# Kernel optimization log

Measured on AMD Instinct MI355X. Metric: run time of the kernel, lower is better.

## Reference

```python
import jax, jax.numpy as jnp
import numpy as np
import math

B, N, H, D = 2, 2048, 16, 64

def setup_inputs() -> dict:
    key = jax.random.key(0)
    kq, kk, kv = jax.random.split(key, 3)
    q = jax.random.normal(kq, (B, N, H, D), dtype=jnp.float32)
    k = jax.random.normal(kk, (B, N, H, D), dtype=jnp.float32)
    v = jax.random.normal(kv, (B, N, H, D), dtype=jnp.float32)
    return {"q": q, "k": k, "v": v}

def reference(q, k, v):
    d = q.shape[-1]
    # [b,n,h,d] -> [b,h,n,d]
    qh = jnp.transpose(q, (0, 2, 1, 3))
    kh = jnp.transpose(k, (0, 2, 1, 3))
    vh = jnp.transpose(v, (0, 2, 1, 3))
    # scores: [b,h,n,n]
    scores = jnp.einsum('bhqd,bhkd->bhqk', qh, kh) / math.sqrt(d)
    # jax.nn.softmax performs the stable max-subtraction internally,
    # matching the original's explicit max-subtract + softmax.
    attn = jax.nn.softmax(scores, axis=-1)
    o = jnp.einsum('bhqk,bhkd->bhqd', attn, vh)
    # back to [b,n,h,d]
    return jnp.transpose(o, (0, 2, 1, 3))
```

## Files before the change

kernel.cpp:

```cpp
#include <hip/hip_runtime.h>


typedef float  f32x4  __attribute__((ext_vector_type(4)));
typedef float  f32x16 __attribute__((ext_vector_type(16)));
typedef short  s16x8  __attribute__((ext_vector_type(8)));
typedef short  s16x4  __attribute__((ext_vector_type(4)));
typedef int    i32x4  __attribute__((ext_vector_type(4)));

#define QSCALE 0.18033688011112042f

__device__ __forceinline__ unsigned short bf16r(float f) {
    unsigned u = __builtin_bit_cast(unsigned, f);
    u += 0x7fffu + ((u >> 16) & 1u);
    return (unsigned short)(u >> 16);
}

__device__ __forceinline__ s16x8 cvt8f_scaled(const float* p, float s) {
    f32x4 a = *(const f32x4*)p;
    f32x4 b = *(const f32x4*)(p + 4);
    s16x8 r;
#pragma unroll
    for (int i = 0; i < 4; ++i) {
        r[i]   = (short)bf16r(a[i] * s);
        r[i+4] = (short)bf16r(b[i] * s);
    }
    return r;
}

__device__ __forceinline__ int cvtpk2(float lo, float hi) {
    int r;
    asm("v_cvt_pk_bf16_f32 %0, %1, %2" : "=v"(r) : "v"(lo), "v"(hi));
    return r;
}

__device__ __forceinline__ void gll16(const unsigned short* g, short* l) {
    __builtin_amdgcn_global_load_lds(
        (const __attribute__((address_space(1))) unsigned int*)g,
        (__attribute__((address_space(3))) unsigned int*)l, 16, 0, 0);
}

__global__ void __launch_bounds__(256)
prep(const float* __restrict__ K, const float* __restrict__ V,
     unsigned short* __restrict__ Kt, unsigned short* __restrict__ Vt) {
    const int t = threadIdx.x, bid = blockIdx.x;
    const int bh = bid & 31, nb = bid >> 5;
    const int b = bh >> 4, h = bh & 15;
    const size_t tile0 = ((size_t)bh * 64 + nb * 2) * 2048;

#pragma unroll
    for (int i = 0; i < 2; ++i) {
        const int lin = i * 256 + t;
        const int kbl = lin >> 8, rem = lin & 255;
        const int kc = rem >> 6, l = rem & 63;
        const int nl = l & 31, gg = l >> 5;
        const float* src = K + ((size_t)(b * 2048 + nb * 64 + kbl * 32 + nl)) * 1024
                             + h * 64 + kc * 16 + gg * 8;
        f32x4 a = *(const f32x4*)src;
        f32x4 c = *(const f32x4*)(src + 4);
        i32x4 o = { cvtpk2(a[0], a[1]), cvtpk2(a[2], a[3]),
                    cvtpk2(c[0], c[1]), cvtpk2(c[2], c[3]) };
        *(i32x4*)(Kt + tile0 + kbl * 2048 + kc * 512 + l * 8) = o;
    }

#pragma unroll
    for (int i = 0; i < 2; ++i) {
        const int lin = i * 256 + t;
        const int kbl = lin >> 8, rem = lin & 255;
        const int qq = rem >> 6, l = rem & 63;
        const int dt = qq >> 1, s = qq & 1;
        const int nl = l & 31, gg = l >> 5;
        const float* vp0 = V + ((size_t)(b * 2048 + nb * 64 + kbl * 32 + 8 * s + 4 * gg)) * 1024
                             + h * 64 + dt * 32 + nl;
        float x0 = vp0[0],     x1 = vp0[1024],  x2 = vp0[2048],  x3 = vp0[3072];
        float x4 = vp0[16384], x5 = vp0[17408], x6 = vp0[18432], x7 = vp0[19456];
        i32x4 o = { cvtpk2(x0, x1), cvtpk2(x2, x3),
                    cvtpk2(x4, x5), cvtpk2(x6, x7) };
        *(i32x4*)(Vt + tile0 + kbl * 2048 + qq * 512 + l * 8) = o;
    }
}

__global__ void __launch_bounds__(256, 3)
attn_fwd(const float* __restrict__ Q, const unsigned short* __restrict__ Kt,
         const unsigned short* __restrict__ Vt, float* __restrict__ O)
{
    __shared__ __align__(16) char smem[52224];

    const int t = threadIdx.x;
    const int ksel = t >> 6, lane = t & 63;
    const int g = lane >> 5, nl = lane & 31;

    const int bid = blockIdx.x;
    const int bh  = bid & 31, qb = bid >> 5;
    const int b   = bh >> 4,  h  = bh & 15;
    const int q0  = qb * 64;

    s16x8 qf[2][4];
#pragma unroll
    for (int qt = 0; qt < 2; ++qt) {
        const float* qp = Q + ((size_t)(b * 2048 + q0 + qt * 32 + nl)) * 1024
                            + h * 64 + g * 8;
#pragma unroll
        for (int kc = 0; kc < 4; ++kc)
            qf[qt][kc] = cvt8f_scaled(qp + kc * 16, QSCALE);
    }
    asm volatile("s_waitcnt vmcnt(0)" ::: "memory");
    __builtin_amdgcn_sched_barrier(0);

    const unsigned short* gk = Kt + (size_t)bh * 131072 + (size_t)ksel * 32768 + lane * 8;
    const unsigned short* gv = Vt + (size_t)bh * 131072 + (size_t)ksel * 32768 + lane * 8;

    short* sK = (short*)(smem + ksel * 8192);
    short* sV = (short*)(smem + ksel * 8192 + 4096);

    f32x16 oa00 = {}, oa01 = {}, oa10 = {}, oa11 = {};
    f32x4  lpv0 = {}, lpv1 = {};

#define ISSUEK(IT) do { const unsigned short* _g = gk + (IT) * 2048;        \
        _Pragma("unroll")                                                   \
        for (int _i = 0; _i < 4; ++_i) gll16(_g + _i * 512, sK + _i * 512); \
        } while (0)
#define ISSUEV(IT) do { const unsigned short* _g = gv + (IT) * 2048;        \
        _Pragma("unroll")                                                   \
        for (int _i = 0; _i < 4; ++_i) gll16(_g + _i * 512, sV + _i * 512); \
        } while (0)
#define WAITV(N) do {                                                       \
        asm volatile("s_waitcnt vmcnt(" #N ")" ::: "memory");               \
        __builtin_amdgcn_sched_barrier(0); } while (0)
#define LGKM0 do {                                                          \
        asm volatile("s_waitcnt lgkmcnt(0)" ::: "memory");                  \
        __builtin_amdgcn_sched_barrier(0); } while (0)

    ISSUEK(0);
    ISSUEV(0);

#pragma unroll
    for (int it = 0; it < 16; ++it) {
        WAITV(4);
        s16x8 kf[4];
#pragma unroll
        for (int kc = 0; kc < 4; ++kc)
            kf[kc] = *(const s16x8*)&sK[kc * 512 + lane * 8];
        LGKM0;
        if (it < 15) ISSUEK(it + 1);

        f32x16 s0 = {}, s1 = {};
#pragma unroll
        for (int kc = 0; kc < 4; ++kc) {
            s0 = __builtin_amdgcn_mfma_f32_32x32x16_bf16(kf[kc], qf[0][kc], s0, 0, 0, 0);
            s1 = __builtin_amdgcn_mfma_f32_32x32x16_bf16(kf[kc], qf[1][kc], s1, 0, 0, 0);
        }
        int pk0[8], pk1[8];
#pragma unroll
        for (int c = 0; c < 4; ++c) {
            f32x4 e0 = { __builtin_amdgcn_exp2f(s0[4*c]),   __builtin_amdgcn_exp2f(s0[4*c+1]),
                         __builtin_amdgcn_exp2f(s0[4*c+2]), __builtin_amdgcn_exp2f(s0[4*c+3]) };
            f32x4 e1 = { __builtin_amdgcn_exp2f(s1[4*c]),   __builtin_amdgcn_exp2f(s1[4*c+1]),
                         __builtin_amdgcn_exp2f(s1[4*c+2]), __builtin_amdgcn_exp2f(s1[4*c+3]) };
            lpv0 += e0; lpv1 += e1;
            pk0[2*c]   = cvtpk2(e0[0], e0[1]);  pk0[2*c+1] = cvtpk2(e0[2], e0[3]);
            pk1[2*c]   = cvtpk2(e1[0], e1[1]);  pk1[2*c+1] = cvtpk2(e1[2], e1[3]);
        }

        if (it < 15) { WAITV(4); } else { WAITV(0); }
        s16x8 vf[4];
#pragma unroll
        for (int qq = 0; qq < 4; ++qq)
            vf[qq] = *(const s16x8*)&sV[qq * 512 + lane * 8];
        LGKM0;
        if (it < 15) ISSUEV(it + 1);

#pragma unroll
        for (int s = 0; s < 2; ++s) {
            i32x4 b0 = { pk0[s*2], pk0[s*2+1], pk0[s*2+4], pk0[s*2+5] };
            i32x4 b1 = { pk1[s*2], pk1[s*2+1], pk1[s*2+4], pk1[s*2+5] };
            s16x8 bb0 = __builtin_bit_cast(s16x8, b0);
            s16x8 bb1 = __builtin_bit_cast(s16x8, b1);
            oa00 = __builtin_amdgcn_mfma_f32_32x32x16_bf16(vf[s],     bb0, oa00, 0, 0, 0);
            oa10 = __builtin_amdgcn_mfma_f32_32x32x16_bf16(vf[2 + s], bb0, oa10, 0, 0, 0);
            oa01 = __builtin_amdgcn_mfma_f32_32x32x16_bf16(vf[s],     bb1, oa01, 0, 0, 0);
            oa11 = __builtin_amdgcn_mfma_f32_32x32x16_bf16(vf[2 + s], bb1, oa11, 0, 0, 0);
        }
    }

#undef ISSUEK
#undef ISSUEV
#undef WAITV
#undef LGKM0

    float lp[2] = { lpv0[0] + lpv0[1] + lpv0[2] + lpv0[3],
                    lpv1[0] + lpv1[1] + lpv1[2] + lpv1[3] };

    __syncthreads();
    float* ex = (float*)smem;
    if (ksel) {
        float* zone = ex + (ksel - 1) * (64 * 68) + lane * 68;
#pragma unroll
        for (int i = 0; i < 4; ++i) {
            *(f32x4*)(zone + i * 4) =
                (f32x4){ oa00[4*i], oa00[4*i+1], oa00[4*i+2], oa00[4*i+3] };
            *(f32x4*)(zone + 16 + i * 4) =
                (f32x4){ oa01[4*i], oa01[4*i+1], oa01[4*i+2], oa01[4*i+3] };
            *(f32x4*)(zone + 32 + i * 4) =
                (f32x4){ oa10[4*i], oa10[4*i+1], oa10[4*i+2], oa10[4*i+3] };
            *(f32x4*)(zone + 48 + i * 4) =
                (f32x4){ oa11[4*i], oa11[4*i+1], oa11[4*i+2], oa11[4*i+3] };
        }
        zone[64] = lp[0];
        zone[65] = lp[1];
    }
    __syncthreads();
    if (!ksel) {
        float lps0 = lp[0], lps1 = lp[1];
#pragma unroll
        for (int z = 0; z < 3; ++z) {
            const float* zn = ex + z * (64 * 68) + lane * 68;
#pragma unroll
            for (int i = 0; i < 4; ++i) {
                f32x4 u0 = *(const f32x4*)(zn + i * 4);
                f32x4 u1 = *(const f32x4*)(zn + 16 + i * 4);
                f32x4 u2 = *(const f32x4*)(zn + 32 + i * 4);
                f32x4 u3 = *(const f32x4*)(zn + 48 + i * 4);
#pragma unroll
                for (int j = 0; j < 4; ++j) {
                    oa00[4*i+j] += u0[j]; oa01[4*i+j] += u1[j];
                    oa10[4*i+j] += u2[j]; oa11[4*i+j] += u3[j];
                }
            }
            lps0 += zn[64];
            lps1 += zn[65];
        }
        float inv[2];
        {
            float ss0 = lps0 + __shfl_xor(lps0, 32);
            float ss1 = lps1 + __shfl_xor(lps1, 32);
            inv[0] = 1.0f / ss0;
            inv[1] = 1.0f / ss1;
        }
        float* op0 = O + ((size_t)(b * 2048 + q0 + nl)) * 1024 + h * 64;
        float* op1 = op0 + 32 * 1024;
#pragma unroll
        for (int rq = 0; rq < 4; ++rq) {
            const int d0 = 8 * rq + 4 * g;
            *(f32x4*)(op0 + d0) = (f32x4){
                oa00[4*rq]   * inv[0], oa00[4*rq+1] * inv[0],
                oa00[4*rq+2] * inv[0], oa00[4*rq+3] * inv[0] };
            *(f32x4*)(op0 + 32 + d0) = (f32x4){
                oa10[4*rq]   * inv[0], oa10[4*rq+1] * inv[0],
                oa10[4*rq+2] * inv[0], oa10[4*rq+3] * inv[0] };
            *(f32x4*)(op1 + d0) = (f32x4){
                oa01[4*rq]   * inv[1], oa01[4*rq+1] * inv[1],
                oa01[4*rq+2] * inv[1], oa01[4*rq+3] * inv[1] };
            *(f32x4*)(op1 + 32 + d0) = (f32x4){
                oa11[4*rq]   * inv[1], oa11[4*rq+1] * inv[1],
                oa11[4*rq+2] * inv[1], oa11[4*rq+3] * inv[1] };
        }
    }
}

extern "C" void kernel_launch(void* const* d_in, const int* in_sizes, int n_in,
                              void* d_out, int out_size, void* d_ws, size_t ws_size,
                              hipStream_t stream) {
    const float* q = (const float*)d_in[0];
    const float* k = (const float*)d_in[1];
    const float* v = (const float*)d_in[2];
    float* o = (float*)d_out;

    unsigned short* Kt = (unsigned short*)d_ws;
    unsigned short* Vt = Kt + 4194304;

    hipLaunchKernelGGL(prep,     dim3(1024), dim3(256), 0, stream, k, v, Kt, Vt);
    hipLaunchKernelGGL(attn_fwd, dim3(1024), dim3(256), 0, stream, q, Kt, Vt, o);
}
```

Baseline: 132.9 us.

## Load K/V fragments directly from global into registers with prefetch and setprio

Replaces the global_load_lds staging of K and V tiles through shared memory with direct global-to-register loads. The next tile is prefetched into registers during the MFMA and exp work, the loop is no longer unrolled, the two score MFMA chains are split into separate blocks, and s_setprio raises wave priority around the MFMA sections. This removes the LDS round trip and its explicit waitcnt fences. In exchange it relies on the compiler's waitcnt placement, increases register pressure, and drops the barrier before the epilogue reuses shared memory.

```diff
diff --git a/kernel.cpp b/kernel.cpp
--- a/kernel.cpp
+++ b/kernel.cpp
@@ -31,12 +31,6 @@
     int r;
     asm("v_cvt_pk_bf16_f32 %0, %1, %2" : "=v"(r) : "v"(lo), "v"(hi));
     return r;
-}
-
-__device__ __forceinline__ void gll16(const unsigned short* g, short* l) {
-    __builtin_amdgcn_global_load_lds(
-        (const __attribute__((address_space(1))) unsigned int*)g,
-        (__attribute__((address_space(3))) unsigned int*)l, 16, 0, 0);
 }
 
 __global__ void __launch_bounds__(256)
@@ -83,7 +77,7 @@
 attn_fwd(const float* __restrict__ Q, const unsigned short* __restrict__ Kt,
          const unsigned short* __restrict__ Vt, float* __restrict__ O)
 {
-    __shared__ __align__(16) char smem[52224];
+    __shared__ __align__(16) float ex[3 * 64 * 68];
 
     const int t = threadIdx.x;
     const int ksel = t >> 6, lane = t & 63;
@@ -103,72 +97,71 @@
         for (int kc = 0; kc < 4; ++kc)
             qf[qt][kc] = cvt8f_scaled(qp + kc * 16, QSCALE);
     }
-    asm volatile("s_waitcnt vmcnt(0)" ::: "memory");
-    __builtin_amdgcn_sched_barrier(0);
-
-    const unsigned short* gk = Kt + (size_t)bh * 131072 + (size_t)ksel * 32768 + lane * 8;
-    const unsigned short* gv = Vt + (size_t)bh * 131072 + (size_t)ksel * 32768 + lane * 8;
-
-    short* sK = (short*)(smem + ksel * 8192);
-    short* sV = (short*)(smem + ksel * 8192 + 4096);
+
+    const unsigned short* ka = Kt + (size_t)bh * 131072 + (size_t)ksel * 32768 + lane * 8;
+    const unsigned short* va = Vt + (size_t)bh * 131072 + (size_t)ksel * 32768 + lane * 8;
 
     f32x16 oa00 = {}, oa01 = {}, oa10 = {}, oa11 = {};
     f32x4  lpv0 = {}, lpv1 = {};
 
-#define ISSUEK(IT) do { const unsigned short* _g = gk + (IT) * 2048;        \
-        _Pragma("unroll")                                                   \
-        for (int _i = 0; _i < 4; ++_i) gll16(_g + _i * 512, sK + _i * 512); \
-        } while (0)
-#define ISSUEV(IT) do { const unsigned short* _g = gv + (IT) * 2048;        \
-        _Pragma("unroll")                                                   \
-        for (int _i = 0; _i < 4; ++_i) gll16(_g + _i * 512, sV + _i * 512); \
-        } while (0)
-#define WAITV(N) do {                                                       \
-        asm volatile("s_waitcnt vmcnt(" #N ")" ::: "memory");               \
-        __builtin_amdgcn_sched_barrier(0); } while (0)
-#define LGKM0 do {                                                          \
-        asm volatile("s_waitcnt lgkmcnt(0)" ::: "memory");                  \
-        __builtin_amdgcn_sched_barrier(0); } while (0)
-
-    ISSUEK(0);
-    ISSUEV(0);
-
-#pragma unroll
+    s16x8 kf[4], vf[4];
+
+#pragma unroll
+    for (int i = 0; i < 4; ++i) {
+        kf[i] = *(const s16x8*)(ka + i * 512);
+        vf[i] = *(const s16x8*)(va + i * 512);
+    }
+    const unsigned short* kp = ka + 2048;
+    const unsigned short* vp = va + 2048;
+
+#pragma unroll 1
     for (int it = 0; it < 16; ++it) {
-        WAITV(4);
-        s16x8 kf[4];
-#pragma unroll
-        for (int kc = 0; kc < 4; ++kc)
-            kf[kc] = *(const s16x8*)&sK[kc * 512 + lane * 8];
-        LGKM0;
-        if (it < 15) ISSUEK(it + 1);
-
-        f32x16 s0 = {}, s1 = {};
-#pragma unroll
-        for (int kc = 0; kc < 4; ++kc) {
-            s0 = __builtin_amdgcn_mfma_f32_32x32x16_bf16(kf[kc], qf[0][kc], s0, 0, 0, 0);
-            s1 = __builtin_amdgcn_mfma_f32_32x32x16_bf16(kf[kc], qf[1][kc], s1, 0, 0, 0);
-        }
         int pk0[8], pk1[8];
-#pragma unroll
-        for (int c = 0; c < 4; ++c) {
-            f32x4 e0 = { __builtin_amdgcn_exp2f(s0[4*c]),   __builtin_amdgcn_exp2f(s0[4*c+1]),
-                         __builtin_amdgcn_exp2f(s0[4*c+2]), __builtin_amdgcn_exp2f(s0[4*c+3]) };
-            f32x4 e1 = { __builtin_amdgcn_exp2f(s1[4*c]),   __builtin_amdgcn_exp2f(s1[4*c+1]),
-                         __builtin_amdgcn_exp2f(s1[4*c+2]), __builtin_amdgcn_exp2f(s1[4*c+3]) };
-            lpv0 += e0; lpv1 += e1;
-            pk0[2*c]   = cvtpk2(e0[0], e0[1]);  pk0[2*c+1] = cvtpk2(e0[2], e0[3]);
-            pk1[2*c]   = cvtpk2(e1[0], e1[1]);  pk1[2*c+1] = cvtpk2(e1[2], e1[3]);
-        }
-
-        if (it < 15) { WAITV(4); } else { WAITV(0); }
-        s16x8 vf[4];
-#pragma unroll
-        for (int qq = 0; qq < 4; ++qq)
-            vf[qq] = *(const s16x8*)&sV[qq * 512 + lane * 8];
-        LGKM0;
-        if (it < 15) ISSUEV(it + 1);
-
+
+        {
+            f32x16 sc = {};
+            __builtin_amdgcn_s_setprio(1);
+#pragma unroll
+            for (int kc = 0; kc < 4; ++kc)
+                sc = __builtin_amdgcn_mfma_f32_32x32x16_bf16(kf[kc], qf[0][kc], sc, 0, 0, 0);
+            __builtin_amdgcn_s_setprio(0);
+#pragma unroll
+            for (int c = 0; c < 4; ++c) {
+                f32x4 e = { __builtin_amdgcn_exp2f(sc[4*c]),
+                            __builtin_amdgcn_exp2f(sc[4*c+1]),
+                            __builtin_amdgcn_exp2f(sc[4*c+2]),
+                            __builtin_amdgcn_exp2f(sc[4*c+3]) };
+                lpv0 += e;
+                pk0[2*c]   = cvtpk2(e[0], e[1]);
+                pk0[2*c+1] = cvtpk2(e[2], e[3]);
+            }
+        }
+
+        {
+            f32x16 sc = {};
+            __builtin_amdgcn_s_setprio(1);
+#pragma unroll
+            for (int kc = 0; kc < 4; ++kc)
+                sc = __builtin_amdgcn_mfma_f32_32x32x16_bf16(kf[kc], qf[1][kc], sc, 0, 0, 0);
+            __builtin_amdgcn_s_setprio(0);
+            if (it < 15) {
+#pragma unroll
+                for (int i = 0; i < 4; ++i)
+                    kf[i] = *(const s16x8*)(kp + i * 512);
+            }
+#pragma unroll
+            for (int c = 0; c < 4; ++c) {
+                f32x4 e = { __builtin_amdgcn_exp2f(sc[4*c]),
+                            __builtin_amdgcn_exp2f(sc[4*c+1]),
+                            __builtin_amdgcn_exp2f(sc[4*c+2]),
+                            __builtin_amdgcn_exp2f(sc[4*c+3]) };
+                lpv1 += e;
+                pk1[2*c]   = cvtpk2(e[0], e[1]);
+                pk1[2*c+1] = cvtpk2(e[2], e[3]);
+            }
+        }
+
+        __builtin_amdgcn_s_setprio(1);
 #pragma unroll
         for (int s = 0; s < 2; ++s) {
             i32x4 b0 = { pk0[s*2], pk0[s*2+1], pk0[s*2+4], pk0[s*2+5] };
@@ -180,18 +173,19 @@
             oa01 = __builtin_amdgcn_mfma_f32_32x32x16_bf16(vf[s],     bb1, oa01, 0, 0, 0);
             oa11 = __builtin_amdgcn_mfma_f32_32x32x16_bf16(vf[2 + s], bb1, oa11, 0, 0, 0);
         }
-    }
-
-#undef ISSUEK
-#undef ISSUEV
-#undef WAITV
-#undef LGKM0
+        __builtin_amdgcn_s_setprio(0);
+        if (it < 15) {
+#pragma unroll
+            for (int i = 0; i < 4; ++i)
+                vf[i] = *(const s16x8*)(vp + i * 512);
+            kp += 2048;
+            vp += 2048;
+        }
+    }
 
     float lp[2] = { lpv0[0] + lpv0[1] + lpv0[2] + lpv0[3],
                     lpv1[0] + lpv1[1] + lpv1[2] + lpv1[3] };
 
-    __syncthreads();
-    float* ex = (float*)smem;
     if (ksel) {
         float* zone = ex + (ksel - 1) * (64 * 68) + lane * 68;
 #pragma unroll
```

Measured after the change: 194.2 us. 1.46x slower.
